# Optimization experiments

Measured on AMD Instinct MI355X. Metric: run time of the kernel, lower is better.

## Reference

```python
import jax, jax.numpy as jnp
import numpy as np

N, E, IN, OUT = 50000, 800000, 256, 256
EPS = 1e-5


def setup_inputs() -> dict:
    key = jax.random.key(0)
    k1, k2, k3 = jax.random.split(key, 3)
    x = jax.random.normal(k1, (N, IN), dtype=jnp.float32)
    edge_index = jax.random.randint(k2, (2, E), 0, N, dtype=jnp.int64)
    batch = jnp.zeros((N,), dtype=jnp.int64)
    # glorot-style init for GCN weight
    scale = jnp.sqrt(2.0 / (IN + OUT)).astype(jnp.float32)
    W = jax.random.normal(k3, (IN, OUT), dtype=jnp.float32) * scale
    conv_bias = jnp.zeros((OUT,), dtype=jnp.float32)
    ln_weight = jnp.ones((OUT,), dtype=jnp.float32)
    ln_bias = jnp.zeros((OUT,), dtype=jnp.float32)
    prelu_a = jnp.full((1,), 0.25, dtype=jnp.float32)  # nn.PReLU default
    return {"x": x, "edge_index": edge_index, "batch": batch, "W": W,
            "conv_bias": conv_bias, "ln_weight": ln_weight,
            "ln_bias": ln_bias, "prelu_a": prelu_a}


def reference(x, edge_index, batch, W, conv_bias, ln_weight, ln_bias, prelu_a):
    n = x.shape[0]
    src, dst = edge_index[0], edge_index[1]
    # GCNConv: add self-loops, symmetric deg^{-1/2} normalization
    loop = jnp.arange(n, dtype=src.dtype)
    src_f = jnp.concatenate([src, loop])  # [E+N]
    dst_f = jnp.concatenate([dst, loop])
    h = x @ W  # [N, OUT] -- transform before propagate (PyG order)
    deg = jax.ops.segment_sum(jnp.ones_like(dst_f, dtype=h.dtype), dst_f,
                              num_segments=n)  # >=1 due to self loops
    dinv = jax.lax.rsqrt(deg)
    norm = dinv[src_f] * dinv[dst_f]  # [E+N]
    out = jax.ops.segment_sum(h[src_f] * norm[:, None], dst_f,
                              num_segments=n) + conv_bias  # [N, OUT]
    # PyG LayerNorm, mode='graph', batch=None: normalize over ALL nodes+feats
    mu = out.mean()
    xc = out - mu
    std = jnp.sqrt((xc * xc).mean())
    y = xc / (std + EPS) * ln_weight + ln_bias
    # PReLU (single shared slope)
    return jnp.where(y >= 0, y, prelu_a * y)
```

## Files before the change

### kernel.cpp

```cpp
#include <hip/hip_runtime.h>
#include <hip/hip_bf16.h>


#define F 256
#define EPSV 1e-5f

typedef __attribute__((ext_vector_type(8))) short short8;
typedef __attribute__((ext_vector_type(4))) float f32x4;

__device__ __forceinline__ unsigned short f2bf(float f) {
  union { float f; unsigned u; } v; v.f = f;
  unsigned r = v.u + 0x7fffu + ((v.u >> 16) & 1u);
  return (unsigned short)(r >> 16);
}

__device__ __forceinline__ float bf2f(unsigned short u) {
  union { unsigned u; float f; } v; v.u = ((unsigned)u) << 16; return v.f;
}


__global__ void init_prep(int* __restrict__ deg_cnt, int N, int NB,
                          const float* __restrict__ W, unsigned short* __restrict__ Wb,
                          int* __restrict__ gbase) {
  if ((int)blockIdx.x < NB) {
    int i = blockIdx.x * 256 + threadIdx.x;
    if (i < N) deg_cnt[i] = 0;
    if (blockIdx.x == 0 && threadIdx.x == 0) *gbase = 0;
    return;
  }
  int gid = (blockIdx.x - NB) * 256 + threadIdx.x;
  int j = gid & 7;
  int lane = (gid >> 3) & 63;
  int kc = (gid >> 9) & 7;
  int tt = gid >> 12;
  int k = kc * 32 + (lane >> 4) * 8 + j;
  int n = tt * 16 + (lane & 15);
  Wb[gid] = f2bf(W[k * 256 + n]);
}


__global__ void count_gemm(const int* __restrict__ dst, int* __restrict__ deg_cnt,
                           int E, int eb,
                           const float* __restrict__ x, const unsigned short* __restrict__ Wb,
                           ushort4* __restrict__ hb, int N) {
  __shared__ unsigned short A[64][264];

  if ((int)blockIdx.x < eb) {
    int e = blockIdx.x * 256 + threadIdx.x;
    if (e < E) atomicAdd(&deg_cnt[dst[e]], 1);
    return;
  }

  int bid = blockIdx.x - eb;
  int m0 = bid * 64;
  int t = threadIdx.x;
  int lane = t & 63;
  int wave = t >> 6;
  int q = lane >> 4;

#pragma unroll
  for (int j = 0; j < 16; ++j) {
    int idx = j * 256 + t;
    int row = idx >> 6;
    int c4 = idx & 63;
    int gr = m0 + row;
    int grc = gr < N ? gr : N - 1;
    f32x4 v = __builtin_nontemporal_load((const f32x4*)(x + (size_t)grc * F + c4 * 4));
    ushort4 u;
    u.x = f2bf(v[0]); u.y = f2bf(v[1]); u.z = f2bf(v[2]); u.w = f2bf(v[3]);
    *(ushort4*)&A[row][c4 * 4] = u;
  }
  __syncthreads();

  f32x4 acc[4][4];
#pragma unroll
  for (int m = 0; m < 4; ++m)
#pragma unroll
    for (int tt = 0; tt < 4; ++tt)
      acc[m][tt] = (f32x4){0.f, 0.f, 0.f, 0.f};

  int arow = lane & 15;
  for (int kc = 0; kc < 8; ++kc) {
    short8 a[4];
#pragma unroll
    for (int m = 0; m < 4; ++m)
      a[m] = *(const short8*)&A[m * 16 + arow][kc * 32 + q * 8];
#pragma unroll
    for (int tt = 0; tt < 4; ++tt) {
      const short8 b = *(const short8*)(Wb + (((wave * 4 + tt) * 8 + kc) * 64 + lane) * 8);
#pragma unroll
      for (int m = 0; m < 4; ++m)
        acc[m][tt] = __builtin_amdgcn_mfma_f32_16x16x32_bf16(a[m], b, acc[m][tt], 0, 0, 0);
    }
  }

  __syncthreads();

  int ccol = lane & 15;
#pragma unroll
  for (int m = 0; m < 4; ++m) {
#pragma unroll
    for (int rr = 0; rr < 4; ++rr) {
      int lrow = m * 16 + q * 4 + rr;
#pragma unroll
      for (int tt = 0; tt < 4; ++tt)
        A[lrow][(wave * 4 + tt) * 16 + ccol] = f2bf(acc[m][tt][rr]);
    }
  }
  __syncthreads();
#pragma unroll
  for (int j = 0; j < 16; ++j) {
    int idx = j * 256 + t;
    int row = idx >> 6;
    int c4 = idx & 63;
    int grow = m0 + row;
    if (grow < N) hb[(size_t)grow * 64 + c4] = *(const ushort4*)&A[row][c4 * 4];
  }
}


__global__ void build_ptr(const int* __restrict__ deg_cnt, float* __restrict__ dinv,
                          int* __restrict__ csr_ptr, int* __restrict__ gbase, int N) {
  __shared__ int s[256];
  __shared__ int base;
  int t = threadIdx.x;
  int i = blockIdx.x * 256 + t;
  int d = (i < N) ? deg_cnt[i] : 0;
  if (i < N) dinv[i] = rsqrtf((float)(d + 1));
  s[t] = d;
  __syncthreads();
  for (int off = 1; off < 256; off <<= 1) {
    int x = (t >= off) ? s[t - off] : 0;
    __syncthreads();
    s[t] += x;
    __syncthreads();
  }
  if (t == 255) base = atomicAdd(gbase, s[255]);
  __syncthreads();
  if (i < N) csr_ptr[i] = base + s[t] - d;
}


__global__ void fill(const int* __restrict__ src, const int* __restrict__ dst,
                     int* __restrict__ csr_ptr, int* __restrict__ csr_src, int E) {
  int e = blockIdx.x * 256 + threadIdx.x;
  if (e < E) {
    int pos = atomicAdd(&csr_ptr[dst[e]], 1);
    csr_src[pos] = src[e];
  }
}


__global__ void aggregate(const ushort4* __restrict__ hb, const int* __restrict__ csr_ptr,
                          const int* __restrict__ deg_cnt, const int* __restrict__ csr_src,
                          const float* __restrict__ dinv, const float* __restrict__ conv_bias,
                          float* __restrict__ out, double2* __restrict__ partials, int N) {
  int wave = threadIdx.x >> 6;
  int lane = threadIdx.x & 63;
  int row = blockIdx.x * 4 + wave;
  float s1 = 0.f, s2 = 0.f;

  if (row < N) {
    float di = dinv[row];
    int b1 = csr_ptr[row];
    int b0 = b1 - deg_cnt[row];
    ushort4 self = hb[(size_t)row * 64 + lane];
    f32x4 acc;
    acc[0] = bf2f(self.x) * di; acc[1] = bf2f(self.y) * di;
    acc[2] = bf2f(self.z) * di; acc[3] = bf2f(self.w) * di;

    for (int e = b0; e < b1; e += 16) {
      int idx[16];
#pragma unroll
      for (int j = 0; j < 16; ++j) {
        int ee = e + j;
        idx[j] = csr_src[ee < b1 ? ee : b1 - 1];
      }
      ushort4 v[16];
#pragma unroll
      for (int j = 0; j < 16; ++j) v[j] = hb[(size_t)idx[j] * 64 + lane];
      float w[16];
#pragma unroll
      for (int j = 0; j < 16; ++j) w[j] = dinv[idx[j]];
#pragma unroll
      for (int j = 0; j < 16; ++j) {
        float m = (e + j < b1) ? w[j] : 0.f;
        acc[0] = fmaf(bf2f(v[j].x), m, acc[0]);
        acc[1] = fmaf(bf2f(v[j].y), m, acc[1]);
        acc[2] = fmaf(bf2f(v[j].z), m, acc[2]);
        acc[3] = fmaf(bf2f(v[j].w), m, acc[3]);
      }
    }

    const f32x4 b = *(const f32x4*)(conv_bias + lane * 4);
    acc[0] = fmaf(acc[0], di, b[0]);
    acc[1] = fmaf(acc[1], di, b[1]);
    acc[2] = fmaf(acc[2], di, b[2]);
    acc[3] = fmaf(acc[3], di, b[3]);
    __builtin_nontemporal_store(acc, (f32x4*)(out + ((size_t)row * 64 + lane) * 4));
    s1 = acc[0] + acc[1] + acc[2] + acc[3];
    s2 = acc[0] * acc[0] + acc[1] * acc[1] + acc[2] * acc[2] + acc[3] * acc[3];
  }

  __shared__ float r1[256];
  __shared__ float r2[256];
  int t = threadIdx.x;
  r1[t] = s1;
  r2[t] = s2;
  __syncthreads();
  for (int off = 128; off > 0; off >>= 1) {
    if (t < off) { r1[t] += r1[t + off]; r2[t] += r2[t + off]; }
    __syncthreads();
  }
  if (t == 0) {
    double2 pp;
    pp.x = (double)r1[0];
    pp.y = (double)r2[0];
    partials[blockIdx.x] = pp;
  }
}


__global__ void norm_prelu(float* __restrict__ out, const double2* __restrict__ partials,
                           int nb, const float* __restrict__ lw, const float* __restrict__ lb,
                           const float* __restrict__ pa, int n4, double cnt) {
  __shared__ double q1[1024];
  __shared__ double q2[1024];
  __shared__ float sstats[2];
  int t = threadIdx.x;
  double a1 = 0.0, a2 = 0.0;
  for (int i = t; i < nb; i += 1024) {
    double2 pp = partials[i];
    a1 += pp.x;
    a2 += pp.y;
  }
  q1[t] = a1;
  q2[t] = a2;
  __syncthreads();
  for (int off = 512; off > 0; off >>= 1) {
    if (t < off) { q1[t] += q1[t + off]; q2[t] += q2[t + off]; }
    __syncthreads();
  }
  if (t == 0) {
    double mu = q1[0] / cnt;
    double var = q2[0] / cnt - mu * mu;
    if (var < 0) var = 0;
    sstats[0] = (float)mu;
    sstats[1] = (float)(1.0 / (sqrt(var) + (double)EPSV));
  }
  __syncthreads();
  float mu = sstats[0];
  float inv = sstats[1];
  float a = pa[0];
  int stride = gridDim.x * 1024;
  for (int i = blockIdx.x * 1024 + t; i < n4; i += stride) {
    int c4 = (i & 63) * 4;
    const f32x4 w = *(const f32x4*)(lw + c4);
    const f32x4 b = *(const f32x4*)(lb + c4);
    f32x4 v = __builtin_nontemporal_load((const f32x4*)(out + (size_t)i * 4));
    f32x4 y;
#pragma unroll
    for (int j = 0; j < 4; ++j) {
      float yv = (v[j] - mu) * inv * w[j] + b[j];
      y[j] = yv >= 0.f ? yv : a * yv;
    }
    __builtin_nontemporal_store(y, (f32x4*)(out + (size_t)i * 4));
  }
}


extern "C" void kernel_launch(void* const* d_in, const int* in_sizes, int n_in,
                              void* d_out, int out_size, void* d_ws, size_t ws_size,
                              hipStream_t stream) {
  const float* x = (const float*)d_in[0];
  const int* eidx = (const int*)d_in[1];
  const float* W = (const float*)d_in[3];
  const float* conv_bias = (const float*)d_in[4];
  const float* ln_w = (const float*)d_in[5];
  const float* ln_b = (const float*)d_in[6];
  const float* prelu_a = (const float*)d_in[7];
  float* out = (float*)d_out;

  int N = in_sizes[0] / F;
  int E = in_sizes[1] / 2;
  const int* src = eidx;
  const int* dst = eidx + E;

  int nAggBlocks = (N + 3) / 4;
  int eb = (E + 255) / 256;
  int gemmb = (N + 63) / 64;
  int NB = (N + 255) / 256;

  char* p = (char*)d_ws;
  auto carve = [&](size_t bytes) { char* r = p; p += (bytes + 255) & ~(size_t)255; return r; };
  ushort4* hb    = (ushort4*)carve((size_t)N * 64 * sizeof(ushort4));
  unsigned short* Wb = (unsigned short*)carve((size_t)F * F * sizeof(short));
  int* deg_cnt   = (int*)carve((size_t)N * sizeof(int));
  float* dinv    = (float*)carve((size_t)N * sizeof(float));
  int* csr_ptr   = (int*)carve((size_t)N * sizeof(int));
  int* csr_src   = (int*)carve((size_t)E * sizeof(int));
  int* gbase     = (int*)carve(sizeof(int));
  double2* partials = (double2*)carve((size_t)nAggBlocks * sizeof(double2));

  init_prep<<<NB + 256, 256, 0, stream>>>(deg_cnt, N, NB, W, Wb, gbase);
  count_gemm<<<eb + gemmb, 256, 0, stream>>>(dst, deg_cnt, E, eb, x, Wb, hb, N);
  build_ptr<<<NB, 256, 0, stream>>>(deg_cnt, dinv, csr_ptr, gbase, N);
  fill<<<eb, 256, 0, stream>>>(src, dst, csr_ptr, csr_src, E);
  aggregate<<<nAggBlocks, 256, 0, stream>>>(hb, csr_ptr, deg_cnt, csr_src, dinv,
                                            conv_bias, out, partials, N);
  int n4 = N * (F / 4);
  norm_prelu<<<256, 1024, 0, stream>>>(out, partials, nAggBlocks, ln_w, ln_b, prelu_a,
                                       n4, (double)N * (double)F);
}
```

Measured before the change: 304.8 us.

## Fuse all GCN stages into one cooperative persistent kernel with grid syncs

Replaces six separate kernel launches with a single cooperative persistent kernel that walks through the stages (weight prep, GEMM plus degree count, scan, CSR fill, aggregate, norm+PReLU) separated by grid.sync. The degree-count atomics now record each edge's rank, so the fill step places edges without a second round of atomics. This is meant to remove launch gaps and per-stage tail effects, at the cost of grid-wide barriers, a persistent grid sized by occupancy (at most 256 CUs times blocks per CU), and a launch-bounds hint that may limit registers for the GEMM and gather loops.

```diff
diff --git a/kernel.cpp b/kernel.cpp
--- a/kernel.cpp
+++ b/kernel.cpp
@@ -1,9 +1,12 @@
 #include <hip/hip_runtime.h>
 #include <hip/hip_bf16.h>
+#include <hip/hip_cooperative_groups.h>
 
 
 #define F 256
 #define EPSV 1e-5f
+
+namespace cg = cooperative_groups;
 
 typedef __attribute__((ext_vector_type(8))) short short8;
 typedef __attribute__((ext_vector_type(4))) float f32x4;
@@ -18,152 +21,139 @@
   union { unsigned u; float f; } v; v.u = ((unsigned)u) << 16; return v.f;
 }
 
-
-__global__ void init_prep(int* __restrict__ deg_cnt, int N, int NB,
-                          const float* __restrict__ W, unsigned short* __restrict__ Wb,
-                          int* __restrict__ gbase) {
-  if ((int)blockIdx.x < NB) {
-    int i = blockIdx.x * 256 + threadIdx.x;
-    if (i < N) deg_cnt[i] = 0;
-    if (blockIdx.x == 0 && threadIdx.x == 0) *gbase = 0;
-    return;
-  }
-  int gid = (blockIdx.x - NB) * 256 + threadIdx.x;
-  int j = gid & 7;
-  int lane = (gid >> 3) & 63;
-  int kc = (gid >> 9) & 7;
-  int tt = gid >> 12;
-  int k = kc * 32 + (lane >> 4) * 8 + j;
-  int n = tt * 16 + (lane & 15);
-  Wb[gid] = f2bf(W[k * 256 + n]);
-}
-
-
-__global__ void count_gemm(const int* __restrict__ dst, int* __restrict__ deg_cnt,
-                           int E, int eb,
-                           const float* __restrict__ x, const unsigned short* __restrict__ Wb,
-                           ushort4* __restrict__ hb, int N) {
+__global__ void __launch_bounds__(256, 4)
+fused(const int* __restrict__ src, const int* __restrict__ dst,
+      const float* __restrict__ x, const float* __restrict__ W,
+      const float* __restrict__ conv_bias, const float* __restrict__ lw,
+      const float* __restrict__ lb, const float* __restrict__ pa,
+      float* __restrict__ out, unsigned short* __restrict__ Wb,
+      ushort4* __restrict__ hb, int* __restrict__ deg_cnt,
+      int* __restrict__ rank, float* __restrict__ dinv,
+      int* __restrict__ csr_ptr, int* __restrict__ csr_src,
+      int* __restrict__ gbase, double2* __restrict__ partials,
+      int N, int E, int NB, int gemmb) {
+  cg::grid_group grid = cg::this_grid();
   __shared__ unsigned short A[64][264];
 
-  if ((int)blockIdx.x < eb) {
-    int e = blockIdx.x * 256 + threadIdx.x;
-    if (e < E) atomicAdd(&deg_cnt[dst[e]], 1);
-    return;
-  }
-
-  int bid = blockIdx.x - eb;
-  int m0 = bid * 64;
-  int t = threadIdx.x;
-  int lane = t & 63;
-  int wave = t >> 6;
-  int q = lane >> 4;
-
-#pragma unroll
-  for (int j = 0; j < 16; ++j) {
-    int idx = j * 256 + t;
-    int row = idx >> 6;
-    int c4 = idx & 63;
-    int gr = m0 + row;
-    int grc = gr < N ? gr : N - 1;
-    f32x4 v = __builtin_nontemporal_load((const f32x4*)(x + (size_t)grc * F + c4 * 4));
-    ushort4 u;
-    u.x = f2bf(v[0]); u.y = f2bf(v[1]); u.z = f2bf(v[2]); u.w = f2bf(v[3]);
-    *(ushort4*)&A[row][c4 * 4] = u;
-  }
-  __syncthreads();
-
-  f32x4 acc[4][4];
-#pragma unroll
-  for (int m = 0; m < 4; ++m)
-#pragma unroll
-    for (int tt = 0; tt < 4; ++tt)
-      acc[m][tt] = (f32x4){0.f, 0.f, 0.f, 0.f};
-
-  int arow = lane & 15;
-  for (int kc = 0; kc < 8; ++kc) {
-    short8 a[4];
+  const int nb = gridDim.x;
+  const int bid = blockIdx.x;
+  const int t = threadIdx.x;
+  const int gsz = nb * 256;
+  const int gtid = bid * 256 + t;
+  const int lane = t & 63;
+  const int wave = t >> 6;
+
+  for (int i = gtid; i < N; i += gsz) deg_cnt[i] = 0;
+  if (gtid == 0) *gbase = 0;
+  for (int gid = gtid; gid < F * F; gid += gsz) {
+    int j = gid & 7;
+    int l = (gid >> 3) & 63;
+    int kc = (gid >> 9) & 7;
+    int tt = gid >> 12;
+    int k = kc * 32 + (l >> 4) * 8 + j;
+    int n = tt * 16 + (l & 15);
+    Wb[gid] = f2bf(W[k * 256 + n]);
+  }
+  grid.sync();
+
+  for (int tile = bid; tile < gemmb; tile += nb) {
+    int m0 = tile * 64;
+    int q = lane >> 4;
+#pragma unroll
+    for (int j = 0; j < 16; ++j) {
+      int idx = j * 256 + t;
+      int row = idx >> 6;
+      int c4 = idx & 63;
+      int gr = m0 + row;
+      int grc = gr < N ? gr : N - 1;
+      f32x4 v = __builtin_nontemporal_load((const f32x4*)(x + (size_t)grc * F + c4 * 4));
+      ushort4 u;
+      u.x = f2bf(v[0]); u.y = f2bf(v[1]); u.z = f2bf(v[2]); u.w = f2bf(v[3]);
+      *(ushort4*)&A[row][c4 * 4] = u;
+    }
+    __syncthreads();
+
+    f32x4 acc[4][4];
 #pragma unroll
     for (int m = 0; m < 4; ++m)
-      a[m] = *(const short8*)&A[m * 16 + arow][kc * 32 + q * 8];
-#pragma unroll
-    for (int tt = 0; tt < 4; ++tt) {
-      const short8 b = *(const short8*)(Wb + (((wave * 4 + tt) * 8 + kc) * 64 + lane) * 8);
+#pragma unroll
+      for (int tt = 0; tt < 4; ++tt)
+        acc[m][tt] = (f32x4){0.f, 0.f, 0.f, 0.f};
+
+    int arow = lane & 15;
+    for (int kc = 0; kc < 8; ++kc) {
+      short8 a[4];
 #pragma unroll
       for (int m = 0; m < 4; ++m)
-        acc[m][tt] = __builtin_amdgcn_mfma_f32_16x16x32_bf16(a[m], b, acc[m][tt], 0, 0, 0);
-    }
-  }
-
-  __syncthreads();
-
-  int ccol = lane & 15;
-#pragma unroll
-  for (int m = 0; m < 4; ++m) {
-#pragma unroll
-    for (int rr = 0; rr < 4; ++rr) {
-      int lrow = m * 16 + q * 4 + rr;
-#pragma unroll
-      for (int tt = 0; tt < 4; ++tt)
-        A[lrow][(wave * 4 + tt) * 16 + ccol] = f2bf(acc[m][tt][rr]);
-    }
-  }
-  __syncthreads();
-#pragma unroll
-  for (int j = 0; j < 16; ++j) {
-    int idx = j * 256 + t;
-    int row = idx >> 6;
-    int c4 = idx & 63;
-    int grow = m0 + row;
-    if (grow < N) hb[(size_t)grow * 64 + c4] = *(const ushort4*)&A[row][c4 * 4];
-  }
-}
-
-
-__global__ void build_ptr(const int* __restrict__ deg_cnt, float* __restrict__ dinv,
-                          int* __restrict__ csr_ptr, int* __restrict__ gbase, int N) {
-  __shared__ int s[256];
-  __shared__ int base;
-  int t = threadIdx.x;
-  int i = blockIdx.x * 256 + t;
-  int d = (i < N) ? deg_cnt[i] : 0;
-  if (i < N) dinv[i] = rsqrtf((float)(d + 1));
-  s[t] = d;
-  __syncthreads();
-  for (int off = 1; off < 256; off <<= 1) {
-    int x = (t >= off) ? s[t - off] : 0;
-    __syncthreads();
-    s[t] += x;
-    __syncthreads();
-  }
-  if (t == 255) base = atomicAdd(gbase, s[255]);
-  __syncthreads();
-  if (i < N) csr_ptr[i] = base + s[t] - d;
-}
-
-
-__global__ void fill(const int* __restrict__ src, const int* __restrict__ dst,
-                     int* __restrict__ csr_ptr, int* __restrict__ csr_src, int E) {
-  int e = blockIdx.x * 256 + threadIdx.x;
-  if (e < E) {
-    int pos = atomicAdd(&csr_ptr[dst[e]], 1);
-    csr_src[pos] = src[e];
-  }
-}
-
-
-__global__ void aggregate(const ushort4* __restrict__ hb, const int* __restrict__ csr_ptr,
-                          const int* __restrict__ deg_cnt, const int* __restrict__ csr_src,
-                          const float* __restrict__ dinv, const float* __restrict__ conv_bias,
-                          float* __restrict__ out, double2* __restrict__ partials, int N) {
-  int wave = threadIdx.x >> 6;
-  int lane = threadIdx.x & 63;
-  int row = blockIdx.x * 4 + wave;
+        a[m] = *(const short8*)&A[m * 16 + arow][kc * 32 + q * 8];
+#pragma unroll
+      for (int tt = 0; tt < 4; ++tt) {
+        const short8 b = *(const short8*)(Wb + (((wave * 4 + tt) * 8 + kc) * 64 + lane) * 8);
+#pragma unroll
+        for (int m = 0; m < 4; ++m)
+          acc[m][tt] = __builtin_amdgcn_mfma_f32_16x16x32_bf16(a[m], b, acc[m][tt], 0, 0, 0);
+      }
+    }
+    __syncthreads();
+
+    int ccol = lane & 15;
+#pragma unroll
+    for (int m = 0; m < 4; ++m) {
+#pragma unroll
+      for (int rr = 0; rr < 4; ++rr) {
+        int lrow = m * 16 + q * 4 + rr;
+#pragma unroll
+        for (int tt = 0; tt < 4; ++tt)
+          A[lrow][(wave * 4 + tt) * 16 + ccol] = f2bf(acc[m][tt][rr]);
+      }
+    }
+    __syncthreads();
+#pragma unroll
+    for (int j = 0; j < 16; ++j) {
+      int idx = j * 256 + t;
+      int row = idx >> 6;
+      int c4 = idx & 63;
+      int grow = m0 + row;
+      if (grow < N) hb[(size_t)grow * 64 + c4] = *(const ushort4*)&A[row][c4 * 4];
+    }
+    __syncthreads();
+  }
+  for (int e = gtid; e < E; e += gsz) rank[e] = atomicAdd(&deg_cnt[dst[e]], 1);
+  grid.sync();
+
+  {
+    int* s = (int*)A;
+    for (int chunk = bid; chunk < NB; chunk += nb) {
+      int i = chunk * 256 + t;
+      int d = (i < N) ? deg_cnt[i] : 0;
+      if (i < N) dinv[i] = rsqrtf((float)(d + 1));
+      s[t] = d;
+      __syncthreads();
+      for (int off = 1; off < 256; off <<= 1) {
+        int xx = (t >= off) ? s[t - off] : 0;
+        __syncthreads();
+        s[t] += xx;
+        __syncthreads();
+      }
+      if (t == 255) s[256] = atomicAdd(gbase, s[255]);
+      __syncthreads();
+      if (i < N) csr_ptr[i] = s[256] + s[t] - d;
+      __syncthreads();
+    }
+  }
+  grid.sync();
+
+  for (int e = gtid; e < E; e += gsz) {
+    int d = dst[e];
+    csr_src[csr_ptr[d] + rank[e]] = src[e];
+  }
+  grid.sync();
+
   float s1 = 0.f, s2 = 0.f;
-
-  if (row < N) {
+  for (int row = bid * 4 + wave; row < N; row += nb * 4) {
     float di = dinv[row];
-    int b1 = csr_ptr[row];
-    int b0 = b1 - deg_cnt[row];
+    int b0 = csr_ptr[row];
+    int b1 = b0 + deg_cnt[row];
     ushort4 self = hb[(size_t)row * 64 + lane];
     f32x4 acc;
     acc[0] = bf2f(self.x) * di; acc[1] = bf2f(self.y) * di;
@@ -198,73 +188,71 @@
     acc[2] = fmaf(acc[2], di, b[2]);
     acc[3] = fmaf(acc[3], di, b[3]);
     __builtin_nontemporal_store(acc, (f32x4*)(out + ((size_t)row * 64 + lane) * 4));
-    s1 = acc[0] + acc[1] + acc[2] + acc[3];
-    s2 = acc[0] * acc[0] + acc[1] * acc[1] + acc[2] * acc[2] + acc[3] * acc[3];
-  }
-
-  __shared__ float r1[256];
-  __shared__ float r2[256];
-  int t = threadIdx.x;
-  r1[t] = s1;
-  r2[t] = s2;
-  __syncthreads();
-  for (int off = 128; off > 0; off >>= 1) {
-    if (t < off) { r1[t] += r1[t + off]; r2[t] += r2[t + off]; }
-    __syncthreads();
-  }
-  if (t == 0) {
-    double2 pp;
-    pp.x = (double)r1[0];
-    pp.y = (double)r2[0];
-    partials[blockIdx.x] = pp;
-  }
-}
-
-
-__global__ void norm_prelu(float* __restrict__ out, const double2* __restrict__ partials,
-                           int nb, const float* __restrict__ lw, const float* __restrict__ lb,
-                           const float* __restrict__ pa, int n4, double cnt) {
-  __shared__ double q1[1024];
-  __shared__ double q2[1024];
-  __shared__ float sstats[2];
-  int t = threadIdx.x;
-  double a1 = 0.0, a2 = 0.0;
-  for (int i = t; i < nb; i += 1024) {
-    double2 pp = partials[i];
-    a1 += pp.x;
-    a2 += pp.y;
-  }
-  q1[t] = a1;
-  q2[t] = a2;
-  __syncthreads();
-  for (int off = 512; off > 0; off >>= 1) {
-    if (t < off) { q1[t] += q1[t + off]; q2[t] += q2[t + off]; }
-    __syncthreads();
-  }
-  if (t == 0) {
-    double mu = q1[0] / cnt;
-    double var = q2[0] / cnt - mu * mu;
-    if (var < 0) var = 0;
-    sstats[0] = (float)mu;
-    sstats[1] = (float)(1.0 / (sqrt(var) + (double)EPSV));
-  }
-  __syncthreads();
-  float mu = sstats[0];
-  float inv = sstats[1];
-  float a = pa[0];
-  int stride = gridDim.x * 1024;
-  for (int i = blockIdx.x * 1024 + t; i < n4; i += stride) {
-    int c4 = (i & 63) * 4;
-    const f32x4 w = *(const f32x4*)(lw + c4);
-    const f32x4 b = *(const f32x4*)(lb + c4);
-    f32x4 v = __builtin_nontemporal_load((const f32x4*)(out + (size_t)i * 4));
-    f32x4 y;
-#pragma unroll
-    for (int j = 0; j < 4; ++j) {
-      float yv = (v[j] - mu) * inv * w[j] + b[j];
-      y[j] = yv >= 0.f ? yv : a * yv;
-    }
-    __builtin_nontemporal_store(y, (f32x4*)(out + (size_t)i * 4));
+    s1 += acc[0] + acc[1] + acc[2] + acc[3];
+    s2 += acc[0] * acc[0] + acc[1] * acc[1] + acc[2] * acc[2] + acc[3] * acc[3];
+  }
+  {
+    float* r1 = (float*)A;
+    float* r2 = r1 + 256;
+    r1[t] = s1;
+    r2[t] = s2;
+    __syncthreads();
+    for (int off = 128; off > 0; off >>= 1) {
+      if (t < off) { r1[t] += r1[t + off]; r2[t] += r2[t + off]; }
+      __syncthreads();
+    }
+    if (t == 0) {
+      double2 pp;
+      pp.x = (double)r1[0];
+      pp.y = (double)r2[0];
+      partials[bid] = pp;
+    }
+  }
+  grid.sync();
+
+  {
+    double* q1 = (double*)A;
+    double* q2 = q1 + 256;
+    double a1 = 0.0, a2 = 0.0;
+    for (int i = t; i < nb; i += 256) {
+      double2 pp = partials[i];
+      a1 += pp.x;
+      a2 += pp.y;
+    }
+    q1[t] = a1;
+    q2[t] = a2;
+    __syncthreads();
+    for (int off = 128; off > 0; off >>= 1) {
+      if (t < off) { q1[t] += q1[t + off]; q2[t] += q2[t + off]; }
+      __syncthreads();
+    }
+    __shared__ float sstats[2];
+    if (t == 0) {
+      double cnt = (double)N * (double)F;
+      double mu = q1[0] / cnt;
+      double var = q2[0] / cnt - mu * mu;
+      if (var < 0) var = 0;
+      sstats[0] = (float)mu;
+      sstats[1] = (float)(1.0 / (sqrt(var) + (double)EPSV));
+    }
+    __syncthreads();
+    float mu = sstats[0];
+    float inv = sstats[1];
+    float a = pa[0];
+    int n4 = N * (F / 4);
+    for (int i = gtid; i < n4; i += gsz) {
+      int c4 = (i & 63) * 4;
+      const f32x4 w = *(const f32x4*)(lw + c4);
+      const f32x4 b = *(const f32x4*)(lb + c4);
+      f32x4 v = __builtin_nontemporal_load((const f32x4*)(out + (size_t)i * 4));
+      f32x4 y;
+#pragma unroll
+      for (int j = 0; j < 4; ++j) {
+        float yv = (v[j] - mu) * inv * w[j] + b[j];
+        y[j] = yv >= 0.f ? yv : a * yv;
+      }
+      __builtin_nontemporal_store(y, (f32x4*)(out + (size_t)i * 4));
+    }
   }
 }
 
@@ -286,8 +274,6 @@
   const int* src = eidx;
   const int* dst = eidx + E;
 
-  int nAggBlocks = (N + 3) / 4;
-  int eb = (E + 255) / 256;
   int gemmb = (N + 63) / 64;
   int NB = (N + 255) / 256;
 
@@ -296,19 +282,28 @@
   ushort4* hb    = (ushort4*)carve((size_t)N * 64 * sizeof(ushort4));
   unsigned short* Wb = (unsigned short*)carve((size_t)F * F * sizeof(short));
   int* deg_cnt   = (int*)carve((size_t)N * sizeof(int));
+  int* rank      = (int*)carve((size_t)E * sizeof(int));
   float* dinv    = (float*)carve((size_t)N * sizeof(float));
   int* csr_ptr   = (int*)carve((size_t)N * sizeof(int));
   int* csr_src   = (int*)carve((size_t)E * sizeof(int));
   int* gbase     = (int*)carve(sizeof(int));
-  double2* partials = (double2*)carve((size_t)nAggBlocks * sizeof(double2));
-
-  init_prep<<<NB + 256, 256, 0, stream>>>(deg_cnt, N, NB, W, Wb, gbase);
-  count_gemm<<<eb + gemmb, 256, 0, stream>>>(dst, deg_cnt, E, eb, x, Wb, hb, N);
-  build_ptr<<<NB, 256, 0, stream>>>(deg_cnt, dinv, csr_ptr, gbase, N);
-  fill<<<eb, 256, 0, stream>>>(src, dst, csr_ptr, csr_src, E);
-  aggregate<<<nAggBlocks, 256, 0, stream>>>(hb, csr_ptr, deg_cnt, csr_src, dinv,
-                                            conv_bias, out, partials, N);
-  int n4 = N * (F / 4);
-  norm_prelu<<<256, 1024, 0, stream>>>(out, partials, nAggBlocks, ln_w, ln_b, prelu_a,
-                                       n4, (double)N * (double)F);
+  double2* partials = (double2*)carve((size_t)4096 * sizeof(double2));
+
+  static int blocksPerCU = 0;
+  if (blocksPerCU == 0) {
+    int maxb = 0;
+    hipError_t err = hipOccupancyMaxActiveBlocksPerMultiprocessor(&maxb, fused, 256, 0);
+    blocksPerCU = (err == hipSuccess && maxb > 0) ? maxb : 4;
+  }
+  int nb = blocksPerCU * 256;
+  if (nb > 4096) nb = 4096;
+
+  void* args[] = {
+    (void*)&src, (void*)&dst, (void*)&x, (void*)&W, (void*)&conv_bias,
+    (void*)&ln_w, (void*)&ln_b, (void*)&prelu_a, (void*)&out, (void*)&Wb,
+    (void*)&hb, (void*)&deg_cnt, (void*)&rank, (void*)&dinv, (void*)&csr_ptr,
+    (void*)&csr_src, (void*)&gbase, (void*)&partials,
+    (void*)&N, (void*)&E, (void*)&NB, (void*)&gemmb
+  };
+  hipLaunchCooperativeKernel((const void*)fused, dim3(nb), dim3(256), args, 0, stream);
 }
```

Result: slower. 615.2 us (+101.8%).

## Split GEMM across count and fill kernels, use atomic ranks for CSR fill

Applied to the files above, without the earlier changes.

The count kernel now records each edge's atomic rank within its destination. The fill step then places edges at csr_ptr+rank with no second round of atomics. The GEMM tiles are split into two halves that co-run with the count and fill phases, overlapping compute with atomic-bound edge work. The stats reduction moves into its own single-block kernel, so each norm_prelu block no longer redoes the partials reduction. This adds an extra E-sized rank buffer and one more launch.

```diff
diff --git a/kernel.cpp b/kernel.cpp
--- a/kernel.cpp
+++ b/kernel.cpp
@@ -39,20 +39,12 @@
 }
 
 
-__global__ void count_gemm(const int* __restrict__ dst, int* __restrict__ deg_cnt,
-                           int E, int eb,
-                           const float* __restrict__ x, const unsigned short* __restrict__ Wb,
-                           ushort4* __restrict__ hb, int N) {
+__device__ __forceinline__ void gemm_tile(int tile, const float* __restrict__ x,
+                                          const unsigned short* __restrict__ Wb,
+                                          ushort4* __restrict__ hb, int N) {
   __shared__ unsigned short A[64][264];
 
-  if ((int)blockIdx.x < eb) {
-    int e = blockIdx.x * 256 + threadIdx.x;
-    if (e < E) atomicAdd(&deg_cnt[dst[e]], 1);
-    return;
-  }
-
-  int bid = blockIdx.x - eb;
-  int m0 = bid * 64;
+  int m0 = tile * 64;
   int t = threadIdx.x;
   int lane = t & 63;
   int wave = t >> 6;
@@ -93,7 +85,6 @@
         acc[m][tt] = __builtin_amdgcn_mfma_f32_16x16x32_bf16(a[m], b, acc[m][tt], 0, 0, 0);
     }
   }
-
   __syncthreads();
 
   int ccol = lane & 15;
@@ -119,10 +110,22 @@
 }
 
 
+__global__ void count_gemmA(const int* __restrict__ dst, int* __restrict__ deg_cnt,
+                            int* __restrict__ rank, int E, int eb,
+                            const float* __restrict__ x, const unsigned short* __restrict__ Wb,
+                            ushort4* __restrict__ hb, int N) {
+  if ((int)blockIdx.x < eb) {
+    int e = blockIdx.x * 256 + threadIdx.x;
+    if (e < E) rank[e] = atomicAdd(&deg_cnt[dst[e]], 1);
+    return;
+  }
+  gemm_tile(blockIdx.x - eb, x, Wb, hb, N);
+}
+
+
 __global__ void build_ptr(const int* __restrict__ deg_cnt, float* __restrict__ dinv,
                           int* __restrict__ csr_ptr, int* __restrict__ gbase, int N) {
-  __shared__ int s[256];
-  __shared__ int base;
+  __shared__ int s[257];
   int t = threadIdx.x;
   int i = blockIdx.x * 256 + t;
   int d = (i < N) ? deg_cnt[i] : 0;
@@ -135,19 +138,26 @@
     s[t] += x;
     __syncthreads();
   }
-  if (t == 255) base = atomicAdd(gbase, s[255]);
-  __syncthreads();
-  if (i < N) csr_ptr[i] = base + s[t] - d;
-}
-
-
-__global__ void fill(const int* __restrict__ src, const int* __restrict__ dst,
-                     int* __restrict__ csr_ptr, int* __restrict__ csr_src, int E) {
-  int e = blockIdx.x * 256 + threadIdx.x;
-  if (e < E) {
-    int pos = atomicAdd(&csr_ptr[dst[e]], 1);
-    csr_src[pos] = src[e];
-  }
+  if (t == 255) s[256] = atomicAdd(gbase, s[255]);
+  __syncthreads();
+  if (i < N) csr_ptr[i] = s[256] + s[t] - d;
+}
+
+
+__global__ void fill_gemmB(const int* __restrict__ src, const int* __restrict__ dst,
+                           const int* __restrict__ rank, const int* __restrict__ csr_ptr,
+                           int* __restrict__ csr_src, int E, int eb, int gA,
+                           const float* __restrict__ x, const unsigned short* __restrict__ Wb,
+                           ushort4* __restrict__ hb, int N) {
+  if ((int)blockIdx.x < eb) {
+    int e = blockIdx.x * 256 + threadIdx.x;
+    if (e < E) {
+      int d = dst[e];
+      csr_src[csr_ptr[d] + rank[e]] = src[e];
+    }
+    return;
+  }
+  gemm_tile(gA + (blockIdx.x - eb), x, Wb, hb, N);
 }
 
 
@@ -162,8 +172,8 @@
 
   if (row < N) {
     float di = dinv[row];
-    int b1 = csr_ptr[row];
-    int b0 = b1 - deg_cnt[row];
+    int b0 = csr_ptr[row];
+    int b1 = b0 + deg_cnt[row];
     ushort4 self = hb[(size_t)row * 64 + lane];
     f32x4 acc;
     acc[0] = bf2f(self.x) * di; acc[1] = bf2f(self.y) * di;
@@ -221,12 +231,10 @@
 }
 
 
-__global__ void norm_prelu(float* __restrict__ out, const double2* __restrict__ partials,
-                           int nb, const float* __restrict__ lw, const float* __restrict__ lb,
-                           const float* __restrict__ pa, int n4, double cnt) {
+__global__ void finalize_stats(const double2* __restrict__ partials, int nb,
+                               float* __restrict__ stats, double cnt) {
   __shared__ double q1[1024];
   __shared__ double q2[1024];
-  __shared__ float sstats[2];
   int t = threadIdx.x;
   double a1 = 0.0, a2 = 0.0;
   for (int i = t; i < nb; i += 1024) {
@@ -245,27 +253,32 @@
     double mu = q1[0] / cnt;
     double var = q2[0] / cnt - mu * mu;
     if (var < 0) var = 0;
-    sstats[0] = (float)mu;
-    sstats[1] = (float)(1.0 / (sqrt(var) + (double)EPSV));
-  }
-  __syncthreads();
-  float mu = sstats[0];
-  float inv = sstats[1];
+    double sd = sqrt(var);
+    stats[0] = (float)mu;
+    stats[1] = (float)(1.0 / (sd + (double)EPSV));
+  }
+}
+
+
+__global__ void norm_prelu(float* __restrict__ out, const float* __restrict__ stats,
+                           const float* __restrict__ lw, const float* __restrict__ lb,
+                           const float* __restrict__ pa, int n4) {
+  int i = blockIdx.x * blockDim.x + threadIdx.x;
+  if (i >= n4) return;
+  float mu = stats[0];
+  float inv = stats[1];
   float a = pa[0];
-  int stride = gridDim.x * 1024;
-  for (int i = blockIdx.x * 1024 + t; i < n4; i += stride) {
-    int c4 = (i & 63) * 4;
-    const f32x4 w = *(const f32x4*)(lw + c4);
-    const f32x4 b = *(const f32x4*)(lb + c4);
-    f32x4 v = __builtin_nontemporal_load((const f32x4*)(out + (size_t)i * 4));
-    f32x4 y;
-#pragma unroll
-    for (int j = 0; j < 4; ++j) {
-      float yv = (v[j] - mu) * inv * w[j] + b[j];
-      y[j] = yv >= 0.f ? yv : a * yv;
-    }
-    __builtin_nontemporal_store(y, (f32x4*)(out + (size_t)i * 4));
-  }
+  int c4 = (i & 63) * 4;
+  const f32x4 w = *(const f32x4*)(lw + c4);
+  const f32x4 b = *(const f32x4*)(lb + c4);
+  f32x4 v = __builtin_nontemporal_load((const f32x4*)(out + (size_t)i * 4));
+  f32x4 y;
+#pragma unroll
+  for (int j = 0; j < 4; ++j) {
+    float yv = (v[j] - mu) * inv * w[j] + b[j];
+    y[j] = yv >= 0.f ? yv : a * yv;
+  }
+  __builtin_nontemporal_store(y, (f32x4*)(out + (size_t)i * 4));
 }
 
 
@@ -289,6 +302,7 @@
   int nAggBlocks = (N + 3) / 4;
   int eb = (E + 255) / 256;
   int gemmb = (N + 63) / 64;
+  int gA = gemmb / 2;
   int NB = (N + 255) / 256;
 
   char* p = (char*)d_ws;
@@ -296,19 +310,23 @@
   ushort4* hb    = (ushort4*)carve((size_t)N * 64 * sizeof(ushort4));
   unsigned short* Wb = (unsigned short*)carve((size_t)F * F * sizeof(short));
   int* deg_cnt   = (int*)carve((size_t)N * sizeof(int));
+  int* rank      = (int*)carve((size_t)E * sizeof(int));
   float* dinv    = (float*)carve((size_t)N * sizeof(float));
   int* csr_ptr   = (int*)carve((size_t)N * sizeof(int));
   int* csr_src   = (int*)carve((size_t)E * sizeof(int));
   int* gbase     = (int*)carve(sizeof(int));
   double2* partials = (double2*)carve((size_t)nAggBlocks * sizeof(double2));
+  float* stats   = (float*)carve(2 * sizeof(float));
 
   init_prep<<<NB + 256, 256, 0, stream>>>(deg_cnt, N, NB, W, Wb, gbase);
-  count_gemm<<<eb + gemmb, 256, 0, stream>>>(dst, deg_cnt, E, eb, x, Wb, hb, N);
+  count_gemmA<<<eb + gA, 256, 0, stream>>>(dst, deg_cnt, rank, E, eb, x, Wb, hb, N);
   build_ptr<<<NB, 256, 0, stream>>>(deg_cnt, dinv, csr_ptr, gbase, N);
-  fill<<<eb, 256, 0, stream>>>(src, dst, csr_ptr, csr_src, E);
+  fill_gemmB<<<eb + (gemmb - gA), 256, 0, stream>>>(src, dst, rank, csr_ptr, csr_src,
+                                                    E, eb, gA, x, Wb, hb, N);
   aggregate<<<nAggBlocks, 256, 0, stream>>>(hb, csr_ptr, deg_cnt, csr_src, dinv,
                                             conv_bias, out, partials, N);
+  finalize_stats<<<1, 1024, 0, stream>>>(partials, nAggBlocks, stats,
+                                         (double)N * (double)F);
   int n4 = N * (F / 4);
-  norm_prelu<<<256, 1024, 0, stream>>>(out, partials, nAggBlocks, ln_w, ln_b, prelu_a,
-                                       n4, (double)N * (double)F);
-}
+  norm_prelu<<<(n4 + 255) / 256, 256, 0, stream>>>(out, stats, ln_w, ln_b, prelu_a, n4);
+}
```

Result: faster. 284.1 us (-6.8%).
